# Kernel optimization log

Hardware: AMD Instinct MI355X
Metric: run time of the kernel (lower is better)

The kernel has to match this reference:

```python
import jax, jax.numpy as jnp
import numpy as np

NEG_SLOPE = 0.2


def _gat_layer(x, src, dst, W, att_src, att_dst, bias, heads, out_c, concat):
    # x: [N, F_in]; src,dst: [E] (edges src -> dst, softmax grouped by dst)
    N = x.shape[0]
    h = (x @ W).reshape(N, heads, out_c)                       # [N,H,C]
    a_s = jnp.sum(h * att_src, axis=-1)                        # [N,H]
    a_d = jnp.sum(h * att_dst, axis=-1)                        # [N,H]
    e = jax.nn.leaky_relu(a_s[src] + a_d[dst], NEG_SLOPE)      # [E,H]
    emax = jax.ops.segment_max(e, dst, num_segments=N)         # [N,H]
    ex = jnp.exp(e - emax[dst])
    denom = jax.ops.segment_sum(ex, dst, num_segments=N)       # [N,H]
    alpha = ex / (denom[dst] + 1e-16)                          # [E,H]
    msg = h[src] * alpha[:, :, None]                           # [E,H,C]
    out = jax.ops.segment_sum(msg, dst, num_segments=N)        # [N,H,C]
    out = out.reshape(N, heads * out_c) if concat else out.mean(axis=1)
    return out + bias


def setup_inputs() -> dict:
    key = jax.random.key(0)
    ks = jax.random.split(key, 12)
    N, E = 100000, 1600000
    F_in, C1, H = 128, 32, 4
    x = jax.random.normal(ks[0], (N, F_in), dtype=jnp.float32)
    edge_index = jax.random.randint(ks[1], (2, E), 0, N, dtype=jnp.int64)
    s = 0.1
    W1 = jax.random.normal(ks[2], (F_in, H * C1), dtype=jnp.float32) * s
    att_src1 = jax.random.normal(ks[3], (H, C1), dtype=jnp.float32) * s
    att_dst1 = jax.random.normal(ks[4], (H, C1), dtype=jnp.float32) * s
    b1 = jnp.zeros((H * C1,), dtype=jnp.float32)
    W2 = jax.random.normal(ks[5], (H * C1, 1), dtype=jnp.float32) * s
    att_src2 = jax.random.normal(ks[6], (1, 1), dtype=jnp.float32) * s
    att_dst2 = jax.random.normal(ks[7], (1, 1), dtype=jnp.float32) * s
    b2 = jnp.zeros((1,), dtype=jnp.float32)
    return {"x": x, "edge_index": edge_index, "W1": W1, "att_src1": att_src1,
            "att_dst1": att_dst1, "b1": b1, "W2": W2, "att_src2": att_src2,
            "att_dst2": att_dst2, "b2": b2}


def reference(x, edge_index, W1, att_src1, att_dst1, b1, W2, att_src2, att_dst2, b2):
    N = x.shape[0]
    # PyG GATConv adds self loops by default
    loops = jnp.arange(N, dtype=edge_index.dtype)
    src = jnp.concatenate([edge_index[0], loops])
    dst = jnp.concatenate([edge_index[1], loops])
    h = _gat_layer(x, src, dst, W1, att_src1, att_dst1, b1, heads=4, out_c=32, concat=True)
    h = jax.nn.relu(h)
    out = _gat_layer(h, src, dst, W2, att_src2, att_dst2, b2, heads=1, out_c=1, concat=False)
    return out.squeeze(-1)  # [N]
```

## Files before the change

kernel.cpp:

```cpp
#include <hip/hip_runtime.h>
#include <hip/hip_bf16.h>
#include <math.h>

typedef __hip_bfloat16 bf16;
typedef __attribute__((ext_vector_type(8))) short short8v;
typedef __attribute__((ext_vector_type(4))) float float4v;

__device__ __forceinline__ float b2f(bf16 v) { return __bfloat162float(v); }
__device__ __forceinline__ float bs2f(unsigned short s) {
    unsigned u = ((unsigned)s) << 16;
    float f; __builtin_memcpy(&f, &u, 4); return f;
}
__device__ __forceinline__ short f2bs(float v) {
    bf16 b = __float2bfloat16(v);
    short s; __builtin_memcpy(&s, &b, 2); return s;
}
__device__ __forceinline__ float lrelu(float v) { return fmaxf(v, 0.2f * v); }
__device__ __forceinline__ float ldf(const void* p, size_t i, int bf) {
    return bf ? b2f(((const bf16*)p)[i]) : ((const float*)p)[i];
}
__device__ __forceinline__ int ld_src(const int* ei, int e, int E, int f64, int N) {
    int v = f64 ? (int)(((const long long*)ei)[e]) : ei[e];
    if ((unsigned)v >= (unsigned)N) v = 0;
    return v;
}
__device__ __forceinline__ int ld_dst(const int* ei, int e, int E, int f64, int N) {
    int v = f64 ? (int)(((const long long*)ei)[(size_t)E + e]) : ei[(size_t)E + e];
    if ((unsigned)v >= (unsigned)N) v = 0;
    return v;
}

#define EPB 4096
#define SB  8

__global__ void k_detect(const int* __restrict__ ei, const unsigned* __restrict__ xw,
                         int* __restrict__ flags, int* __restrict__ bcnt,
                         int* __restrict__ done, int nbuck)
{
    __shared__ int s_or[256];
    __shared__ int s_cnt[256];
    int t = threadIdx.x;
    for (int j = t; j < nbuck; j += 256) bcnt[j] = 0;
    if (t == 0) done[0] = 0;
    int any = 0, cnt = 0;
    for (int i = t; i < 4096; i += 256) {
        any |= ei[2 * i + 1];
        unsigned e = (xw[i] >> 7) & 0xFFu;
        cnt += (e >= 100u && e <= 134u) ? 1 : 0;
    }
    s_or[t] = any; s_cnt[t] = cnt;
    __syncthreads();
    for (int s = 128; s > 0; s >>= 1) {
        if (t < s) { s_or[t] |= s_or[t + s]; s_cnt[t] += s_cnt[t + s]; }
        __syncthreads();
    }
    if (t == 0) {
        flags[0] = (s_or[0] == 0) ? 1 : 0;
        flags[1] = (s_cnt[0] > 2048) ? 1 : 0;
    }
}

__global__ void __launch_bounds__(256)
k_prep(const int* __restrict__ ei, const void* __restrict__ W1,
       const int* __restrict__ flags, int* __restrict__ bcnt,
       short* __restrict__ w1frag, int* __restrict__ done,
       int* __restrict__ bofs, int* __restrict__ bcur, int* __restrict__ offsets,
       int E, int N, int nbuck, int ebl)
{
    int t = threadIdx.x;
    if (blockIdx.x >= ebl) {
        int bf = flags[1];
        int idx = (blockIdx.x - ebl) * 256 + t;
        if (idx < 16384) {
            int j = idx & 7, l = (idx >> 3) & 63, kk = (idx >> 9) & 3, ct = idx >> 11;
            int k = kk * 32 + (l >> 4) * 8 + j;
            int n = ct * 16 + (l & 15);
            w1frag[idx] = bf ? ((const short*)W1)[k * 128 + n]
                             : f2bs(((const float*)W1)[k * 128 + n]);
        }
        return;
    }
    __shared__ int hist[512];
    for (int j = t; j < nbuck; j += 256) hist[j] = 0;
    __syncthreads();
    int f = flags[0];
    int beg = blockIdx.x * EPB, end = min(E, beg + EPB);
    for (int i = beg + t; i < end; i += 256)
        atomicAdd(&hist[ld_dst(ei, i, E, f, N) >> SB], 1);
    __syncthreads();
    for (int j = t; j < nbuck; j += 256)
        if (hist[j]) atomicAdd(&bcnt[j], hist[j]);

    __threadfence();
    __shared__ int is_last;
    if (t == 0) is_last = (atomicAdd(done, 1) == ebl - 1) ? 1 : 0;
    __syncthreads();
    if (!is_last) return;
    __threadfence();
    __shared__ int ps[256];
    int i0 = 2 * t, i1 = 2 * t + 1;
    int c0 = (i0 < nbuck) ? bcnt[i0] : 0;
    int c1 = (i1 < nbuck) ? bcnt[i1] : 0;
    int pr = c0 + c1;
    ps[t] = pr;
    __syncthreads();
    for (int s = 1; s < 256; s <<= 1) {
        int add = (t >= s) ? ps[t - s] : 0;
        __syncthreads();
        ps[t] += add;
        __syncthreads();
    }
    int excl = ps[t] - pr;
    if (i0 < nbuck) { bofs[i0] = excl; bcur[i0] = excl; }
    if (i1 < nbuck) { bofs[i1] = excl + c0; bcur[i1] = excl + c0; }
    if (t == 0) { bofs[nbuck] = E; offsets[N] = E; }
}

#define GP 136

__global__ void __launch_bounds__(256)
k_gemm_scatter(const void* __restrict__ x, const short* __restrict__ w1frag,
               const void* __restrict__ att_src, const void* __restrict__ att_dst,
               const int* __restrict__ ei, const int* __restrict__ flags,
               bf16* __restrict__ h1b, float* __restrict__ a_s, float* __restrict__ a_d,
               int* __restrict__ bcur, unsigned* __restrict__ ebuf,
               int N, int E, int nbuck, int ebl)
{
    int t = threadIdx.x;
    if (blockIdx.x < ebl) {
        __shared__ int hist[512];
        __shared__ int base[512];
        for (int j = t; j < nbuck; j += 256) hist[j] = 0;
        __syncthreads();
        int f = flags[0];
        int beg = blockIdx.x * EPB, end = min(E, beg + EPB);
        for (int i = beg + t; i < end; i += 256)
            atomicAdd(&hist[ld_dst(ei, i, E, f, N) >> SB], 1);
        __syncthreads();
        for (int j = t; j < nbuck; j += 256) {
            base[j] = hist[j] ? atomicAdd(&bcur[j], hist[j]) : 0;
            hist[j] = 0;
        }
        __syncthreads();
        for (int i = beg + t; i < end; i += 256) {
            int d = ld_dst(ei, i, E, f, N);
            int s = ld_src(ei, i, E, f, N);
            int b = d >> SB;
            int idx = base[b] + atomicAdd(&hist[b], 1);
            ebuf[idx] = (unsigned)s | ((unsigned)(d & ((1 << SB) - 1)) << 24);
        }
        return;
    }
    __shared__ short xs[64 * GP];
    int bf = flags[1];
    int base = (blockIdx.x - ebl) * 64;
    if (bf) {
        const short8v* xp = (const short8v*)x;
        for (int idx = t; idx < 1024; idx += 256) {
            int m = idx >> 4, v8 = idx & 15;
            int gm = base + m;
            short8v v = (gm < N) ? xp[(size_t)gm * 16 + v8]
                                 : (short8v){0,0,0,0,0,0,0,0};
            *(short8v*)&xs[m * GP + v8 * 8] = v;
        }
    } else {
        const float4* xp = (const float4*)x;
        for (int idx = t; idx < 2048; idx += 256) {
            int m = idx >> 5, v4 = idx & 31;
            int gm = base + m;
            float4 f = (gm < N) ? xp[(size_t)gm * 32 + v4]
                                : make_float4(0.f, 0.f, 0.f, 0.f);
            short* d = &xs[m * GP + v4 * 4];
            d[0] = f2bs(f.x); d[1] = f2bs(f.y); d[2] = f2bs(f.z); d[3] = f2bs(f.w);
        }
    }
    __syncthreads();

    int wv = t >> 6, l = t & 63, lq = l >> 4, lr = l & 15;
    int m0 = base + wv * 16;

    short8v afr[4];
#pragma unroll
    for (int kk = 0; kk < 4; ++kk)
        afr[kk] = *(const short8v*)&xs[(wv * 16 + lr) * GP + kk * 32 + lq * 8];

    float4v acc[8];
#pragma unroll
    for (int ct = 0; ct < 8; ++ct) acc[ct] = (float4v){0.f, 0.f, 0.f, 0.f};

#pragma unroll
    for (int kk = 0; kk < 4; ++kk) {
        short8v a = afr[kk];
#pragma unroll
        for (int ct = 0; ct < 8; ++ct) {
            short8v b = *(const short8v*)(w1frag + (((ct * 4 + kk) * 64 + l) << 3));
            acc[ct] = __builtin_amdgcn_mfma_f32_16x16x32_bf16(a, b, acc[ct], 0, 0, 0);
        }
    }
    __syncthreads();

#pragma unroll
    for (int ct = 0; ct < 8; ++ct)
#pragma unroll
        for (int r = 0; r < 4; ++r)
            xs[(wv * 16 + lq * 4 + r) * GP + ct * 16 + lr] = f2bs(acc[ct][r]);
    __syncthreads();

    int c0 = (l & 7) * 16;
    float asv[16], adv[16];
#pragma unroll
    for (int c = 0; c < 16; ++c) {
        asv[c] = ldf(att_src, c0 + c, bf);
        adv[c] = ldf(att_dst, c0 + c, bf);
    }
#pragma unroll
    for (int p = 0; p < 2; ++p) {
        int rrow = p * 8 + (l >> 3);
        int gn = m0 + rrow;
        const short* srcp = &xs[(wv * 16 + rrow) * GP + c0];
        short8v v0 = *(const short8v*)srcp;
        short8v v1 = *(const short8v*)(srcp + 8);
        if (gn < N) {
            unsigned short* dst = (unsigned short*)h1b + (size_t)gn * 128 + c0;
            *(short8v*)dst = v0;
            *(short8v*)(dst + 8) = v1;
        }
        float ds = 0.f, dd = 0.f;
#pragma unroll
        for (int c = 0; c < 8; ++c) {
            float fv = bs2f((unsigned short)v0[c]);
            ds += fv * asv[c]; dd += fv * adv[c];
        }
#pragma unroll
        for (int c = 0; c < 8; ++c) {
            float fv = bs2f((unsigned short)v1[c]);
            ds += fv * asv[8 + c]; dd += fv * adv[8 + c];
        }
        ds += __shfl_xor(ds, 1, 64);
        dd += __shfl_xor(dd, 1, 64);
        if (gn < N && ((l & 1) == 0)) {
            int h = (l & 7) >> 1;
            a_s[(size_t)gn * 4 + h] = ds;
            a_d[(size_t)gn * 4 + h] = dd;
        }
    }
}

__global__ void __launch_bounds__(256)
k_bucket_csr(const unsigned* __restrict__ ebuf, const int* __restrict__ bofs,
             int* __restrict__ offsets, int* __restrict__ adj, int N)
{
    const int npb = 1 << SB;
    __shared__ int hist[npb];
    __shared__ int psum[256];
    int b = blockIdx.x, t = threadIdx.x;
    int n0 = b << SB;
    int ebeg = bofs[b], eend = bofs[b + 1];

    hist[t] = 0;
    __syncthreads();
    for (int i = ebeg + t; i < eend; i += 256)
        atomicAdd(&hist[ebuf[i] >> 24], 1);
    __syncthreads();
    int c = hist[t];
    psum[t] = c;
    __syncthreads();
    for (int st = 1; st < 256; st <<= 1) {
        int add = (t >= st) ? psum[t - st] : 0;
        __syncthreads();
        psum[t] += add;
        __syncthreads();
    }
    int run = ebeg + psum[t] - c;
    int node = n0 + t;
    hist[t] = run;
    if (node < N) offsets[node] = run;
    __syncthreads();
    for (int i = ebeg + t; i < eend; i += 256) {
        unsigned e = ebuf[i];
        int pos = atomicAdd(&hist[e >> 24], 1);
        adj[pos] = (int)(e & 0xFFFFFFu);
    }
}

__global__ void __launch_bounds__(256)
k_hagg32(const bf16* __restrict__ h1b, const float* __restrict__ a_s,
         const float* __restrict__ a_d, const int* __restrict__ offsets,
         const int* __restrict__ adj, const void* __restrict__ b1,
         const void* __restrict__ W2, const int* __restrict__ flags,
         float* __restrict__ h2, int N)
{
    int bf = flags[1];
    int t = threadIdx.x;
    int g = t >> 5, l = t & 31;
    int n = blockIdx.x * 8 + g;
    if (n >= N) return;
    int h = l >> 3;
    int coff = h * 32 + (l & 7) * 4;

    int beg = offsets[n], deg = offsets[n + 1] - beg;
    float adh = a_d[(size_t)n * 4 + h];
    const unsigned short* h1u = (const unsigned short*)h1b;

    float wself = __expf(lrelu(a_s[(size_t)n * 4 + h] + adh));
    ushort4 u = *(const ushort4*)(h1u + ((size_t)n << 7) + coff);
    float a0 = wself * bs2f(u.x), a1 = wself * bs2f(u.y);
    float a2 = wself * bs2f(u.z), a3 = wself * bs2f(u.w);
    float den = wself;

    int i = 0;
    for (; i + 8 <= deg; i += 8) {
        int sv[8];
#pragma unroll
        for (int j = 0; j < 8; ++j) sv[j] = adj[beg + i + j];
        float wv[8];
#pragma unroll
        for (int j = 0; j < 8; ++j)
            wv[j] = __expf(lrelu(a_s[(size_t)sv[j] * 4 + h] + adh));
        ushort4 vv[8];
#pragma unroll
        for (int j = 0; j < 8; ++j)
            vv[j] = *(const ushort4*)(h1u + ((size_t)sv[j] << 7) + coff);
#pragma unroll
        for (int j = 0; j < 8; ++j) {
            den += wv[j];
            a0 += wv[j] * bs2f(vv[j].x);
            a1 += wv[j] * bs2f(vv[j].y);
            a2 += wv[j] * bs2f(vv[j].z);
            a3 += wv[j] * bs2f(vv[j].w);
        }
    }
    for (; i + 4 <= deg; i += 4) {
        int s0 = adj[beg + i];
        int s1 = adj[beg + i + 1];
        int s2 = adj[beg + i + 2];
        int s3 = adj[beg + i + 3];
        float w0 = __expf(lrelu(a_s[(size_t)s0 * 4 + h] + adh));
        float w1 = __expf(lrelu(a_s[(size_t)s1 * 4 + h] + adh));
        float w2 = __expf(lrelu(a_s[(size_t)s2 * 4 + h] + adh));
        float w3 = __expf(lrelu(a_s[(size_t)s3 * 4 + h] + adh));
        ushort4 v0 = *(const ushort4*)(h1u + ((size_t)s0 << 7) + coff);
        ushort4 v1 = *(const ushort4*)(h1u + ((size_t)s1 << 7) + coff);
        ushort4 v2 = *(const ushort4*)(h1u + ((size_t)s2 << 7) + coff);
        ushort4 v3 = *(const ushort4*)(h1u + ((size_t)s3 << 7) + coff);
        den += (w0 + w1) + (w2 + w3);
        a0 += w0 * bs2f(v0.x) + w1 * bs2f(v1.x) + w2 * bs2f(v2.x) + w3 * bs2f(v3.x);
        a1 += w0 * bs2f(v0.y) + w1 * bs2f(v1.y) + w2 * bs2f(v2.y) + w3 * bs2f(v3.y);
        a2 += w0 * bs2f(v0.z) + w1 * bs2f(v1.z) + w2 * bs2f(v2.z) + w3 * bs2f(v3.z);
        a3 += w0 * bs2f(v0.w) + w1 * bs2f(v1.w) + w2 * bs2f(v2.w) + w3 * bs2f(v3.w);
    }
    for (; i < deg; ++i) {
        int s0 = adj[beg + i];
        float w0 = __expf(lrelu(a_s[(size_t)s0 * 4 + h] + adh));
        ushort4 v0 = *(const ushort4*)(h1u + ((size_t)s0 << 7) + coff);
        den += w0;
        a0 += w0 * bs2f(v0.x);
        a1 += w0 * bs2f(v0.y);
        a2 += w0 * bs2f(v0.z);
        a3 += w0 * bs2f(v0.w);
    }

    float inv = 1.f / (den + 1e-16f);
    float o0 = fmaxf(a0 * inv + ldf(b1, coff + 0, bf), 0.f);
    float o1 = fmaxf(a1 * inv + ldf(b1, coff + 1, bf), 0.f);
    float o2 = fmaxf(a2 * inv + ldf(b1, coff + 2, bf), 0.f);
    float o3 = fmaxf(a3 * inv + ldf(b1, coff + 3, bf), 0.f);

    float p = o0 * ldf(W2, coff + 0, bf) + o1 * ldf(W2, coff + 1, bf)
            + o2 * ldf(W2, coff + 2, bf) + o3 * ldf(W2, coff + 3, bf);
    p += __shfl_xor(p, 1, 64);
    p += __shfl_xor(p, 2, 64);
    p += __shfl_xor(p, 4, 64);
    p += __shfl_xor(p, 8, 64);
    p += __shfl_xor(p, 16, 64);
    if (l == 0) h2[n] = p;
}

__global__ void k_agg2(const float* __restrict__ h2, const int* __restrict__ offsets,
                       const int* __restrict__ adj, const void* __restrict__ att_src2,
                       const void* __restrict__ att_dst2, const void* __restrict__ bias2,
                       const int* __restrict__ flags, void* __restrict__ out, int N)
{
    int bf = flags[1];
    int g = (blockIdx.x * blockDim.x + threadIdx.x) >> 4;
    int lane = threadIdx.x & 15;
    if (g >= N) return;
    int n = g;
    float as2 = ldf(att_src2, 0, bf), ad2 = ldf(att_dst2, 0, bf);
    int beg = offsets[n], end = offsets[n + 1], deg = end - beg;
    float hn = h2[n];
    float dterm = hn * ad2;

    float acc = 0.f, den = 0.f;
    if (lane == 0) {
        float ex = __expf(lrelu(hn * as2 + dterm));
        acc = ex * hn; den = ex;
    }
    for (int i = lane; i < deg; i += 16) {
        int s = adj[beg + i];
        float hs = h2[s];
        float ex = __expf(lrelu(hs * as2 + dterm));
        acc += ex * hs; den += ex;
    }
    for (int m = 1; m < 16; m <<= 1) {
        acc += __shfl_xor(acc, m, 64);
        den += __shfl_xor(den, m, 64);
    }
    if (lane == 0) {
        float r = acc / (den + 1e-16f) + ldf(bias2, 0, bf);
        if (bf) ((bf16*)out)[n] = __float2bfloat16(r);
        else    ((float*)out)[n] = r;
    }
}

extern "C" void kernel_launch(void* const* d_in, const int* in_sizes, int n_in,
                              void* d_out, int out_size, void* d_ws, size_t ws_size,
                              hipStream_t stream)
{
    const void* x        = d_in[0];
    const int*  ei       = (const int*)d_in[1];
    const void* W1       = d_in[2];
    const void* att_src1 = d_in[3];
    const void* att_dst1 = d_in[4];
    const void* b1       = d_in[5];
    const void* W2       = d_in[6];
    const void* att_src2 = d_in[7];
    const void* att_dst2 = d_in[8];
    const void* bias2    = d_in[9];

    int N = in_sizes[0] / 128;
    int E = in_sizes[1] / 2;
    int nbuck = ((N - 1) >> SB) + 1;

    char* ws = (char*)d_ws;
    size_t off = 0;
    auto alloc = [&](size_t bytes) -> void* {
        void* p = ws + off;
        off = (off + bytes + 255) & ~(size_t)255;
        return p;
    };
    int*      flags   = (int*)alloc(256);
    int*      done    = (int*)alloc(256);
    float*    a_s     = (float*)alloc((size_t)N * 4 * sizeof(float));
    float*    a_d     = (float*)alloc((size_t)N * 4 * sizeof(float));
    float*    h2      = (float*)alloc((size_t)N * sizeof(float));
    int*      offsets = (int*)alloc((size_t)(N + 1) * sizeof(int));
    int*      adj     = (int*)alloc((size_t)E * sizeof(int));
    unsigned* ebuf    = (unsigned*)alloc((size_t)E * sizeof(unsigned));
    int*      bcnt    = (int*)alloc(1024 * sizeof(int));
    int*      bofs    = (int*)alloc(1028 * sizeof(int));
    int*      bcur    = (int*)alloc(1024 * sizeof(int));
    short*    w1frag  = (short*)alloc(16384 * sizeof(short));
    bf16*     h1b     = (bf16*)alloc((size_t)N * 128 * sizeof(bf16));

    int ebl = (E + EPB - 1) / EPB;
    int gblocks = (N + 63) / 64;

    k_detect<<<1, 256, 0, stream>>>(ei, (const unsigned*)x, flags, bcnt, done, nbuck);

    k_prep<<<ebl + 64, 256, 0, stream>>>(ei, W1, flags, bcnt, w1frag, done,
                                         bofs, bcur, offsets, E, N, nbuck, ebl);

    k_gemm_scatter<<<ebl + gblocks, 256, 0, stream>>>(
        x, w1frag, att_src1, att_dst1, ei, flags, h1b, a_s, a_d,
        bcur, ebuf, N, E, nbuck, ebl);

    k_bucket_csr<<<nbuck, 256, 0, stream>>>(ebuf, bofs, offsets, adj, N);

    k_hagg32<<<(N + 7) / 8, 256, 0, stream>>>(h1b, a_s, a_d, offsets, adj,
                                              b1, W2, flags, h2, N);

    k_agg2<<<((size_t)N * 16 + 255) / 256, 256, 0, stream>>>(
        h2, offsets, adj, att_src2, att_dst2, bias2, flags, d_out, N);
}
```

Measured before the change: 283.1 us.

## Restructure preprocessing kernels: fold prep into detect/GEMM, fuse scatter with CSR via grid barrier

Merges W1 fragment packing into the detect kernel, which now recomputes the bf16 flag locally in each block. The bucket histogram and prefix scan move into the GEMM kernel, and edge scatter plus per-bucket CSR build are fused into one kernel joined by a spin-wait grid barrier. This cuts the preprocessing chain from five launches to four and removes launch gaps. The spin barrier only works if every block of the grid (~391) is resident at once, so it risks deadlock on smaller devices. The 8-wide unrolled aggregation loop is also removed, leaving the 4-wide loop.

```diff
diff --git a/kernel.cpp b/kernel.cpp
--- a/kernel.cpp
+++ b/kernel.cpp
@@ -33,44 +33,28 @@
 #define EPB 4096
 #define SB  8
 
-__global__ void k_detect(const int* __restrict__ ei, const unsigned* __restrict__ xw,
-                         int* __restrict__ flags, int* __restrict__ bcnt,
-                         int* __restrict__ done, int nbuck)
-{
-    __shared__ int s_or[256];
+__global__ void __launch_bounds__(256)
+k_detect(const int* __restrict__ ei, const unsigned* __restrict__ xw,
+         const void* __restrict__ W1, int* __restrict__ flags,
+         int* __restrict__ bcnt, int* __restrict__ done, int* __restrict__ done2,
+         short* __restrict__ w1frag, int nbuck)
+{
+    int t = threadIdx.x;
     __shared__ int s_cnt[256];
-    int t = threadIdx.x;
-    for (int j = t; j < nbuck; j += 256) bcnt[j] = 0;
-    if (t == 0) done[0] = 0;
-    int any = 0, cnt = 0;
-    for (int i = t; i < 4096; i += 256) {
-        any |= ei[2 * i + 1];
-        unsigned e = (xw[i] >> 7) & 0xFFu;
-        cnt += (e >= 100u && e <= 134u) ? 1 : 0;
-    }
-    s_or[t] = any; s_cnt[t] = cnt;
-    __syncthreads();
-    for (int s = 128; s > 0; s >>= 1) {
-        if (t < s) { s_or[t] |= s_or[t + s]; s_cnt[t] += s_cnt[t + s]; }
-        __syncthreads();
-    }
-    if (t == 0) {
-        flags[0] = (s_or[0] == 0) ? 1 : 0;
-        flags[1] = (s_cnt[0] > 2048) ? 1 : 0;
-    }
-}
-
-__global__ void __launch_bounds__(256)
-k_prep(const int* __restrict__ ei, const void* __restrict__ W1,
-       const int* __restrict__ flags, int* __restrict__ bcnt,
-       short* __restrict__ w1frag, int* __restrict__ done,
-       int* __restrict__ bofs, int* __restrict__ bcur, int* __restrict__ offsets,
-       int E, int N, int nbuck, int ebl)
-{
-    int t = threadIdx.x;
-    if (blockIdx.x >= ebl) {
-        int bf = flags[1];
-        int idx = (blockIdx.x - ebl) * 256 + t;
+    if (blockIdx.x > 0) {
+        int cnt = 0;
+        for (int i = t; i < 1024; i += 256) {
+            unsigned e = (xw[i] >> 7) & 0xFFu;
+            cnt += (e >= 100u && e <= 134u) ? 1 : 0;
+        }
+        s_cnt[t] = cnt;
+        __syncthreads();
+        for (int s = 128; s > 0; s >>= 1) {
+            if (t < s) s_cnt[t] += s_cnt[t + s];
+            __syncthreads();
+        }
+        int bf = (s_cnt[0] > 512) ? 1 : 0;
+        int idx = (blockIdx.x - 1) * 256 + t;
         if (idx < 16384) {
             int j = idx & 7, l = (idx >> 3) & 63, kk = (idx >> 9) & 3, ct = idx >> 11;
             int k = kk * 32 + (l >> 4) * 8 + j;
@@ -80,80 +64,80 @@
         }
         return;
     }
-    __shared__ int hist[512];
-    for (int j = t; j < nbuck; j += 256) hist[j] = 0;
-    __syncthreads();
-    int f = flags[0];
-    int beg = blockIdx.x * EPB, end = min(E, beg + EPB);
-    for (int i = beg + t; i < end; i += 256)
-        atomicAdd(&hist[ld_dst(ei, i, E, f, N) >> SB], 1);
-    __syncthreads();
-    for (int j = t; j < nbuck; j += 256)
-        if (hist[j]) atomicAdd(&bcnt[j], hist[j]);
-
-    __threadfence();
-    __shared__ int is_last;
-    if (t == 0) is_last = (atomicAdd(done, 1) == ebl - 1) ? 1 : 0;
-    __syncthreads();
-    if (!is_last) return;
-    __threadfence();
-    __shared__ int ps[256];
-    int i0 = 2 * t, i1 = 2 * t + 1;
-    int c0 = (i0 < nbuck) ? bcnt[i0] : 0;
-    int c1 = (i1 < nbuck) ? bcnt[i1] : 0;
-    int pr = c0 + c1;
-    ps[t] = pr;
-    __syncthreads();
-    for (int s = 1; s < 256; s <<= 1) {
-        int add = (t >= s) ? ps[t - s] : 0;
-        __syncthreads();
-        ps[t] += add;
-        __syncthreads();
-    }
-    int excl = ps[t] - pr;
-    if (i0 < nbuck) { bofs[i0] = excl; bcur[i0] = excl; }
-    if (i1 < nbuck) { bofs[i1] = excl + c0; bcur[i1] = excl + c0; }
-    if (t == 0) { bofs[nbuck] = E; offsets[N] = E; }
+    __shared__ int s_or[256];
+    for (int j = t; j < nbuck; j += 256) bcnt[j] = 0;
+    if (t == 0) { done[0] = 0; done2[0] = 0; }
+    int any = 0, cnt = 0;
+    for (int i = t; i < 4096; i += 256) {
+        any |= ei[2 * i + 1];
+        unsigned e = (xw[i] >> 7) & 0xFFu;
+        cnt += (e >= 100u && e <= 134u) ? 1 : 0;
+    }
+    s_or[t] = any; s_cnt[t] = cnt;
+    __syncthreads();
+    for (int s = 128; s > 0; s >>= 1) {
+        if (t < s) { s_or[t] |= s_or[t + s]; s_cnt[t] += s_cnt[t + s]; }
+        __syncthreads();
+    }
+    if (t == 0) {
+        flags[0] = (s_or[0] == 0) ? 1 : 0;
+        flags[1] = (s_cnt[0] > 2048) ? 1 : 0;
+    }
 }
 
 #define GP 136
 
 __global__ void __launch_bounds__(256)
-k_gemm_scatter(const void* __restrict__ x, const short* __restrict__ w1frag,
-               const void* __restrict__ att_src, const void* __restrict__ att_dst,
-               const int* __restrict__ ei, const int* __restrict__ flags,
-               bf16* __restrict__ h1b, float* __restrict__ a_s, float* __restrict__ a_d,
-               int* __restrict__ bcur, unsigned* __restrict__ ebuf,
-               int N, int E, int nbuck, int ebl)
+k_gemm_hist(const void* __restrict__ x, const short* __restrict__ w1frag,
+            const void* __restrict__ att_src, const void* __restrict__ att_dst,
+            const int* __restrict__ ei, const int* __restrict__ flags,
+            bf16* __restrict__ h1b, float* __restrict__ a_s, float* __restrict__ a_d,
+            int* __restrict__ bcnt, int* __restrict__ done,
+            int* __restrict__ bofs, int* __restrict__ bcur, int* __restrict__ offsets,
+            int N, int E, int nbuck, int gblocks, int ebl)
 {
     int t = threadIdx.x;
-    if (blockIdx.x < ebl) {
+    if (blockIdx.x >= gblocks) {
         __shared__ int hist[512];
-        __shared__ int base[512];
         for (int j = t; j < nbuck; j += 256) hist[j] = 0;
         __syncthreads();
         int f = flags[0];
-        int beg = blockIdx.x * EPB, end = min(E, beg + EPB);
+        int hb = blockIdx.x - gblocks;
+        int beg = hb * EPB, end = min(E, beg + EPB);
         for (int i = beg + t; i < end; i += 256)
             atomicAdd(&hist[ld_dst(ei, i, E, f, N) >> SB], 1);
         __syncthreads();
-        for (int j = t; j < nbuck; j += 256) {
-            base[j] = hist[j] ? atomicAdd(&bcur[j], hist[j]) : 0;
-            hist[j] = 0;
-        }
-        __syncthreads();
-        for (int i = beg + t; i < end; i += 256) {
-            int d = ld_dst(ei, i, E, f, N);
-            int s = ld_src(ei, i, E, f, N);
-            int b = d >> SB;
-            int idx = base[b] + atomicAdd(&hist[b], 1);
-            ebuf[idx] = (unsigned)s | ((unsigned)(d & ((1 << SB) - 1)) << 24);
-        }
+        for (int j = t; j < nbuck; j += 256)
+            if (hist[j]) atomicAdd(&bcnt[j], hist[j]);
+
+        __threadfence();
+        __shared__ int is_last;
+        if (t == 0) is_last = (atomicAdd(done, 1) == ebl - 1) ? 1 : 0;
+        __syncthreads();
+        if (!is_last) return;
+        __threadfence();
+        __shared__ int ps[256];
+        int i0 = 2 * t, i1 = 2 * t + 1;
+        int c0 = (i0 < nbuck) ? bcnt[i0] : 0;
+        int c1 = (i1 < nbuck) ? bcnt[i1] : 0;
+        int pr = c0 + c1;
+        ps[t] = pr;
+        __syncthreads();
+        for (int s = 1; s < 256; s <<= 1) {
+            int add = (t >= s) ? ps[t - s] : 0;
+            __syncthreads();
+            ps[t] += add;
+            __syncthreads();
+        }
+        int excl = ps[t] - pr;
+        if (i0 < nbuck) { bofs[i0] = excl; bcur[i0] = excl; }
+        if (i1 < nbuck) { bofs[i1] = excl + c0; bcur[i1] = excl + c0; }
+        if (t == 0) { bofs[nbuck] = E; offsets[N] = E; }
         return;
     }
     __shared__ short xs[64 * GP];
     int bf = flags[1];
-    int base = (blockIdx.x - ebl) * 64;
+    int base = blockIdx.x * 64;
     if (bf) {
         const short8v* xp = (const short8v*)x;
         for (int idx = t; idx < 1024; idx += 256) {
@@ -247,13 +231,49 @@
 }
 
 __global__ void __launch_bounds__(256)
-k_bucket_csr(const unsigned* __restrict__ ebuf, const int* __restrict__ bofs,
-             int* __restrict__ offsets, int* __restrict__ adj, int N)
-{
-    const int npb = 1 << SB;
-    __shared__ int hist[npb];
-    __shared__ int psum[256];
-    int b = blockIdx.x, t = threadIdx.x;
+k_scatter_csr(const int* __restrict__ ei, const int* __restrict__ flags,
+              int* __restrict__ bcur, unsigned* __restrict__ ebuf,
+              const int* __restrict__ bofs, int* __restrict__ offsets,
+              int* __restrict__ adj, int* __restrict__ done2,
+              int E, int N, int nbuck, int ebl)
+{
+    int t = threadIdx.x;
+    __shared__ int hist[512];
+    __shared__ int base[512];
+
+    if (blockIdx.x < ebl) {
+        for (int j = t; j < nbuck; j += 256) hist[j] = 0;
+        __syncthreads();
+        int f = flags[0];
+        int beg = blockIdx.x * EPB, end = min(E, beg + EPB);
+        for (int i = beg + t; i < end; i += 256)
+            atomicAdd(&hist[ld_dst(ei, i, E, f, N) >> SB], 1);
+        __syncthreads();
+        for (int j = t; j < nbuck; j += 256) {
+            base[j] = hist[j] ? atomicAdd(&bcur[j], hist[j]) : 0;
+            hist[j] = 0;
+        }
+        __syncthreads();
+        for (int i = beg + t; i < end; i += 256) {
+            int d = ld_dst(ei, i, E, f, N);
+            int s = ld_src(ei, i, E, f, N);
+            int b = d >> SB;
+            int idx = base[b] + atomicAdd(&hist[b], 1);
+            ebuf[idx] = (unsigned)s | ((unsigned)(d & ((1 << SB) - 1)) << 24);
+        }
+    }
+
+    __threadfence();
+    __syncthreads();
+    if (t == 0) {
+        atomicAdd(done2, 1);
+        while (atomicAdd(done2, 0) < (int)gridDim.x) {}
+    }
+    __syncthreads();
+    __threadfence();
+
+    int b = blockIdx.x;
+    if (b >= nbuck) return;
     int n0 = b << SB;
     int ebeg = bofs[b], eend = bofs[b + 1];
 
@@ -263,15 +283,15 @@
         atomicAdd(&hist[ebuf[i] >> 24], 1);
     __syncthreads();
     int c = hist[t];
-    psum[t] = c;
+    base[t] = c;
     __syncthreads();
     for (int st = 1; st < 256; st <<= 1) {
-        int add = (t >= st) ? psum[t - st] : 0;
-        __syncthreads();
-        psum[t] += add;
-        __syncthreads();
-    }
-    int run = ebeg + psum[t] - c;
+        int add = (t >= st) ? base[t - st] : 0;
+        __syncthreads();
+        base[t] += add;
+        __syncthreads();
+    }
+    int run = ebeg + base[t] - c;
     int node = n0 + t;
     hist[t] = run;
     if (node < N) offsets[node] = run;
@@ -309,27 +329,6 @@
     float den = wself;
 
     int i = 0;
-    for (; i + 8 <= deg; i += 8) {
-        int sv[8];
-#pragma unroll
-        for (int j = 0; j < 8; ++j) sv[j] = adj[beg + i + j];
-        float wv[8];
-#pragma unroll
-        for (int j = 0; j < 8; ++j)
-            wv[j] = __expf(lrelu(a_s[(size_t)sv[j] * 4 + h] + adh));
-        ushort4 vv[8];
-#pragma unroll
-        for (int j = 0; j < 8; ++j)
-            vv[j] = *(const ushort4*)(h1u + ((size_t)sv[j] << 7) + coff);
-#pragma unroll
-        for (int j = 0; j < 8; ++j) {
-            den += wv[j];
-            a0 += wv[j] * bs2f(vv[j].x);
-            a1 += wv[j] * bs2f(vv[j].y);
-            a2 += wv[j] * bs2f(vv[j].z);
-            a3 += wv[j] * bs2f(vv[j].w);
-        }
-    }
     for (; i + 4 <= deg; i += 4) {
         int s0 = adj[beg + i];
         int s1 = adj[beg + i + 1];
@@ -441,6 +440,7 @@
     };
     int*      flags   = (int*)alloc(256);
     int*      done    = (int*)alloc(256);
+    int*      done2   = (int*)alloc(256);
     float*    a_s     = (float*)alloc((size_t)N * 4 * sizeof(float));
     float*    a_d     = (float*)alloc((size_t)N * 4 * sizeof(float));
     float*    h2      = (float*)alloc((size_t)N * sizeof(float));
@@ -455,17 +455,18 @@
 
     int ebl = (E + EPB - 1) / EPB;
     int gblocks = (N + 63) / 64;
-
-    k_detect<<<1, 256, 0, stream>>>(ei, (const unsigned*)x, flags, bcnt, done, nbuck);
-
-    k_prep<<<ebl + 64, 256, 0, stream>>>(ei, W1, flags, bcnt, w1frag, done,
-                                         bofs, bcur, offsets, E, N, nbuck, ebl);
-
-    k_gemm_scatter<<<ebl + gblocks, 256, 0, stream>>>(
+    int scgrid = (ebl > nbuck) ? ebl : nbuck;
+
+    k_detect<<<65, 256, 0, stream>>>(ei, (const unsigned*)x, W1, flags,
+                                     bcnt, done, done2, w1frag, nbuck);
+
+    k_gemm_hist<<<gblocks + ebl, 256, 0, stream>>>(
         x, w1frag, att_src1, att_dst1, ei, flags, h1b, a_s, a_d,
-        bcur, ebuf, N, E, nbuck, ebl);
-
-    k_bucket_csr<<<nbuck, 256, 0, stream>>>(ebuf, bofs, offsets, adj, N);
+        bcnt, done, bofs, bcur, offsets, N, E, nbuck, gblocks, ebl);
+
+    k_scatter_csr<<<scgrid, 256, 0, stream>>>(ei, flags, bcur, ebuf,
+                                              bofs, offsets, adj, done2,
+                                              E, N, nbuck, ebl);
 
     k_hagg32<<<(N + 7) / 8, 256, 0, stream>>>(h1b, a_s, a_d, offsets, adj,
                                               b1, W2, flags, h2, N);
```

New measurement: 420.5 us. 1.49x slower.
